# Kernel tuning notes

Measured on AMD Instinct MI355X. Metric: run time of the kernel, lower is better.

The kernel has to match this reference:

```python
import jax, jax.numpy as jnp
import numpy as np

N_BASES = 4  # a,c,g,u
L = 4096


def setup_inputs() -> dict:
    key = jax.random.key(0)
    seq_ids = jax.random.randint(key, (L,), 0, N_BASES, dtype=jnp.int64)
    # BASE_DICT: each base -> one-hot vector of length N_BASES (identity table)
    base_table = jnp.eye(N_BASES, dtype=jnp.float32)
    return {"seq_ids": seq_ids, "base_table": base_table}


def reference(seq_ids, base_table):
    # one_hot[i] = BASE_DICT[sequence[i]]  -> (L, N_BASES)
    one_hot = base_table[seq_ids]
    n = one_hot.shape[0]
    # ret[:, i, j] = cat(one_hot[i], one_hot[j])
    row = jnp.broadcast_to(one_hot[:, None, :], (n, n, N_BASES))  # first half, varies with i
    col = jnp.broadcast_to(one_hot[None, :, :], (n, n, N_BASES))  # second half, varies with j
    ret = jnp.concatenate([row, col], axis=-1)        # (L, L, 2*N_BASES)
    ret = jnp.transpose(ret, (2, 0, 1))               # (2*N_BASES, L, L)
    return ret[None]                                  # (1, 2*N_BASES, L, L)
```

## Files before the change

### kernel.cpp

```cpp
#include <hip/hip_runtime.h>
#include <hip/hip_bf16.h>


#define L 4096
#define TOTAL_F4 (8u * L * L / 4u)

typedef float v4f __attribute__((ext_vector_type(4)));
typedef int   v4i __attribute__((ext_vector_type(4)));

__global__ __launch_bounds__(256) void SequenceEmbedding_30923764532139_kernel(
        const int* __restrict__ seq,
        const float* __restrict__ table,
        v4f* __restrict__ out) {
    unsigned idx = blockIdx.x * blockDim.x + threadIdx.x;
    unsigned e = idx << 2;
    unsigned c = e >> 24;
    unsigned i = (e >> 12) & (L - 1);
    unsigned j = e & (L - 1);

    v4f val;
    if (c < 4u) {
        float x = table[(unsigned)seq[i] * 4u + c];
        val = (v4f){x, x, x, x};
    } else {
        unsigned cc = c - 4u;
        v4i s = *(const v4i*)(seq + j);
        val.x = table[(unsigned)s.x * 4u + cc];
        val.y = table[(unsigned)s.y * 4u + cc];
        val.z = table[(unsigned)s.z * 4u + cc];
        val.w = table[(unsigned)s.w * 4u + cc];
    }
    __builtin_nontemporal_store(val, out + idx);
}

extern "C" void kernel_launch(void* const* d_in, const int* in_sizes, int n_in,
                              void* d_out, int out_size, void* d_ws, size_t ws_size,
                              hipStream_t stream) {
    const int*   seq   = (const int*)d_in[0];
    const float* table = (const float*)d_in[1];
    v4f*         out   = (v4f*)d_out;

    dim3 block(256);
    dim3 grid(TOTAL_F4 / 256u);
    SequenceEmbedding_30923764532139_kernel<<<grid, block, 0, stream>>>(seq, table, out);
}
```

Measured before the change: 512.4 us.

## Process four full rows per block and reuse computed values across rows

Each block now covers four output rows of one channel plane, with each thread writing 16 float4s instead of one. Row-broadcast planes look up the table value once per row. Column planes compute the four j-vectors once and reuse them for all four rows. This cuts the grid size and the per-element index and gather work, at the cost of more work per thread. The kernel stays bound by the output stores.

```diff
diff --git a/kernel.cpp b/kernel.cpp
--- a/kernel.cpp
+++ b/kernel.cpp
@@ -1,9 +1,10 @@
 #include <hip/hip_runtime.h>
-#include <hip/hip_bf16.h>
 
 
 #define L 4096
-#define TOTAL_F4 (8u * L * L / 4u)
+#define ROWS 4
+#define ROW_F4 (L / 4)
+#define PLANE_F4 (L * (L / 4))
 
 typedef float v4f __attribute__((ext_vector_type(4)));
 typedef int   v4i __attribute__((ext_vector_type(4)));
@@ -12,25 +13,49 @@
         const int* __restrict__ seq,
         const float* __restrict__ table,
         v4f* __restrict__ out) {
-    unsigned idx = blockIdx.x * blockDim.x + threadIdx.x;
-    unsigned e = idx << 2;
-    unsigned c = e >> 24;
-    unsigned i = (e >> 12) & (L - 1);
-    unsigned j = e & (L - 1);
+    const unsigned bid   = blockIdx.x;
+    const unsigned plane = bid >> 10;
+    const unsigned i0    = (bid & 1023u) * ROWS;
+    const unsigned t     = threadIdx.x;
 
-    v4f val;
-    if (c < 4u) {
-        float x = table[(unsigned)seq[i] * 4u + c];
-        val = (v4f){x, x, x, x};
+    v4f* base = out + (size_t)plane * PLANE_F4 + (size_t)i0 * ROW_F4;
+
+    if (plane < 4u) {
+        const unsigned c = plane;
+        float x[ROWS];
+#pragma unroll
+        for (int r = 0; r < ROWS; ++r)
+            x[r] = table[(unsigned)seq[i0 + r] * 4u + c];
+
+#pragma unroll
+        for (int r = 0; r < ROWS; ++r) {
+            const v4f val = (v4f){x[r], x[r], x[r], x[r]};
+            v4f* rowp = base + (size_t)r * ROW_F4;
+#pragma unroll
+            for (int k = 0; k < 4; ++k)
+                __builtin_nontemporal_store(val, rowp + (unsigned)k * 256u + t);
+        }
     } else {
-        unsigned cc = c - 4u;
-        v4i s = *(const v4i*)(seq + j);
-        val.x = table[(unsigned)s.x * 4u + cc];
-        val.y = table[(unsigned)s.y * 4u + cc];
-        val.z = table[(unsigned)s.z * 4u + cc];
-        val.w = table[(unsigned)s.w * 4u + cc];
+        const unsigned cc = plane - 4u;
+        v4f vals[4];
+#pragma unroll
+        for (int k = 0; k < 4; ++k) {
+            const unsigned j = (unsigned)k * 1024u + t * 4u;
+            const v4i s = *(const v4i*)(seq + j);
+            vals[k].x = table[(unsigned)s.x * 4u + cc];
+            vals[k].y = table[(unsigned)s.y * 4u + cc];
+            vals[k].z = table[(unsigned)s.z * 4u + cc];
+            vals[k].w = table[(unsigned)s.w * 4u + cc];
+        }
+
+#pragma unroll
+        for (int r = 0; r < ROWS; ++r) {
+            v4f* rowp = base + (size_t)r * ROW_F4;
+#pragma unroll
+            for (int k = 0; k < 4; ++k)
+                __builtin_nontemporal_store(vals[k], rowp + (unsigned)k * 256u + t);
+        }
     }
-    __builtin_nontemporal_store(val, out + idx);
 }
 
 extern "C" void kernel_launch(void* const* d_in, const int* in_sizes, int n_in,
@@ -41,6 +66,6 @@
     v4f*         out   = (v4f*)d_out;
 
     dim3 block(256);
-    dim3 grid(TOTAL_F4 / 256u);
+    dim3 grid(8u * (L / ROWS));
     SequenceEmbedding_30923764532139_kernel<<<grid, block, 0, stream>>>(seq, table, out);
 }
```

New measurement: 529.6 us. +3.3%, slower.
